# Kernel optimization log

Hardware: AMD Instinct MI355X
Metric: run time of the kernel (lower is better)

Reference implementation:

```python
import jax, jax.numpy as jnp
import numpy as np

B, C, H, W = 4, 64, 128, 128
KS = 3
N = KS * KS  # 9 sampling points per output pixel


def conv2d(x, w, stride=1, pad=0):
    return jax.lax.conv_general_dilated(
        x, w, (stride, stride), ((pad, pad), (pad, pad)),
        dimension_numbers=('NCHW', 'OIHW', 'NCHW'))


def deform_conv(x, w_p, b_p, w_m, b_m, w_c):
    """Modulated deformable conv (DCNv2, pure-pytorch DeformConv2d semantics)."""
    b, c, h, w = x.shape
    # offset: (B, 2N, H, W); mask: (B, N, H, W)
    off = conv2d(x, w_p, pad=1) + b_p[None, :, None, None]
    m = jax.nn.sigmoid(conv2d(x, w_m, pad=1) + b_m[None, :, None, None])
    # zero-pad input (padding=1), sampling coords live in padded frame
    xp = jnp.pad(x, ((0, 0), (0, 0), (1, 1), (1, 1)))
    hp, wp = h + 2, w + 2
    r = (KS - 1) // 2
    pn_x, pn_y = jnp.meshgrid(jnp.arange(-r, r + 1, dtype=x.dtype),
                              jnp.arange(-r, r + 1, dtype=x.dtype), indexing='ij')
    pn_x, pn_y = pn_x.reshape(-1), pn_y.reshape(-1)        # (N,)
    p0_x = jnp.arange(1, h + 1, dtype=x.dtype)[:, None, None]  # (H,1,1)
    p0_y = jnp.arange(1, w + 1, dtype=x.dtype)[None, :, None]  # (1,W,1)
    off_x = jnp.transpose(off[:, :N], (0, 2, 3, 1))        # (B,H,W,N)
    off_y = jnp.transpose(off[:, N:], (0, 2, 3, 1))
    px = p0_x + pn_x + off_x                               # (B,H,W,N)
    py = p0_y + pn_y + off_y
    fx, fy = jnp.floor(px), jnp.floor(py)
    q_lt_x = jnp.clip(fx, 0, hp - 1)
    q_lt_y = jnp.clip(fy, 0, wp - 1)
    q_rb_x = jnp.clip(fx + 1, 0, hp - 1)
    q_rb_y = jnp.clip(fy + 1, 0, wp - 1)
    pxc = jnp.clip(px, 0, hp - 1)
    pyc = jnp.clip(py, 0, wp - 1)
    g_lt = (1 + (q_lt_x - pxc)) * (1 + (q_lt_y - pyc))
    g_rb = (1 - (q_rb_x - pxc)) * (1 - (q_rb_y - pyc))
    g_lb = (1 + (q_lt_x - pxc)) * (1 - (q_rb_y - pyc))
    g_rt = (1 - (q_rb_x - pxc)) * (1 + (q_lt_y - pyc))
    xf = xp.reshape(b, c, hp * wp)

    def gather(xb, ix, iy):
        idx = ix.astype(jnp.int32) * wp + iy.astype(jnp.int32)  # (H,W,N)
        return xb[:, idx]                                       # (C,H,W,N)

    v_lt = jax.vmap(gather)(xf, q_lt_x, q_lt_y)
    v_rb = jax.vmap(gather)(xf, q_rb_x, q_rb_y)
    v_lb = jax.vmap(gather)(xf, q_lt_x, q_rb_y)
    v_rt = jax.vmap(gather)(xf, q_rb_x, q_lt_y)
    x_off = (g_lt[:, None] * v_lt + g_rb[:, None] * v_rb
             + g_lb[:, None] * v_lb + g_rt[:, None] * v_rt)   # (B,C,H,W,N)
    x_off = x_off * jnp.transpose(m, (0, 2, 3, 1))[:, None]   # modulation
    # (B,C,H,W,ki,kj) -> (B,C,H*KS,W*KS), then conv k=KS stride=KS, no bias
    x_off = x_off.reshape(b, c, h, w, KS, KS).transpose(0, 1, 2, 4, 3, 5)
    x_off = x_off.reshape(b, c, h * KS, w * KS)
    return conv2d(x_off, w_c, stride=KS, pad=0)


def setup_inputs() -> dict:
    key = jax.random.key(0)
    ks = jax.random.split(key, 12)
    w_scale = 1.0 / np.sqrt(C * KS * KS)
    d = {'x': jax.random.normal(ks[0], (B, C, H, W), jnp.float32)}
    for i, pre in enumerate(['d1_', 'd2_']):
        o = 1 + i * 5
        d[pre + 'w_p'] = jax.random.normal(ks[o], (2 * N, C, 3, 3), jnp.float32) * 0.02
        d[pre + 'b_p'] = jnp.zeros((2 * N,), jnp.float32)
        d[pre + 'w_m'] = jax.random.normal(ks[o + 1], (N, C, 3, 3), jnp.float32) * 0.02
        d[pre + 'b_m'] = jnp.zeros((N,), jnp.float32)
        d[pre + 'w_c'] = jax.random.normal(ks[o + 2], (C, C, KS, KS), jnp.float32) * w_scale
    return d


def reference(x, d1_w_p, d1_b_p, d1_w_m, d1_b_m, d1_w_c,
              d2_w_p, d2_b_p, d2_w_m, d2_b_m, d2_w_c):
    y = deform_conv(x, d1_w_p, d1_b_p, d1_w_m, d1_b_m, d1_w_c)
    y = jax.nn.relu(y)
    y = deform_conv(y, d2_w_p, d2_b_p, d2_w_m, d2_b_m, d2_w_c)
    return y + x
```

## Files before the change

### kernel.cpp

```cpp
#include <hip/hip_runtime.h>
#include <hip/hip_bf16.h>
#include <math.h>

typedef __attribute__((ext_vector_type(8))) short short8;
typedef __attribute__((ext_vector_type(16))) float f32x16;
typedef unsigned int uint;
typedef unsigned short ushort;

#define HWSZ 16384
#define PADW 130
#define SLAB (PADW*PADW*64)
#define WR 15
#define WC 23
#define NCELL (WR*WC)
#define CSTRIDE 144
#define OMS_OFF (NCELL*CSTRIDE)
#define SM_BYTES (OMS_OFF + 4*27*33*4)

__device__ __forceinline__ uint pk2bf(float a, float b) {
    union { __hip_bfloat162 h; uint u; } cv;
    cv.h = __float22bfloat162_rn(make_float2(a, b)); return cv.u;
}
__device__ __forceinline__ float bflo(uint u){ return __uint_as_float(u << 16); }
__device__ __forceinline__ float bfhi(uint u){ return __uint_as_float(u & 0xffff0000u); }

__device__ __forceinline__ short8 combine4(short8 s0, short8 s1, short8 s2, short8 s3,
                                           float g0, float g1, float g2, float g3)
{
    uint4 u0 = *(uint4*)&s0, u1 = *(uint4*)&s1, u2 = *(uint4*)&s2, u3 = *(uint4*)&s3;
    float v0,v1,v2,v3,v4,v5,v6,v7;
    v0 = g0*bflo(u0.x); v1 = g0*bfhi(u0.x); v2 = g0*bflo(u0.y); v3 = g0*bfhi(u0.y);
    v4 = g0*bflo(u0.z); v5 = g0*bfhi(u0.z); v6 = g0*bflo(u0.w); v7 = g0*bfhi(u0.w);
    v0 = fmaf(g1,bflo(u1.x),v0); v1 = fmaf(g1,bfhi(u1.x),v1);
    v2 = fmaf(g1,bflo(u1.y),v2); v3 = fmaf(g1,bfhi(u1.y),v3);
    v4 = fmaf(g1,bflo(u1.z),v4); v5 = fmaf(g1,bfhi(u1.z),v5);
    v6 = fmaf(g1,bflo(u1.w),v6); v7 = fmaf(g1,bfhi(u1.w),v7);
    v0 = fmaf(g2,bflo(u2.x),v0); v1 = fmaf(g2,bfhi(u2.x),v1);
    v2 = fmaf(g2,bflo(u2.y),v2); v3 = fmaf(g2,bfhi(u2.y),v3);
    v4 = fmaf(g2,bflo(u2.z),v4); v5 = fmaf(g2,bfhi(u2.z),v5);
    v6 = fmaf(g2,bflo(u2.w),v6); v7 = fmaf(g2,bfhi(u2.w),v7);
    v0 = fmaf(g3,bflo(u3.x),v0); v1 = fmaf(g3,bfhi(u3.x),v1);
    v2 = fmaf(g3,bflo(u3.y),v2); v3 = fmaf(g3,bfhi(u3.y),v3);
    v4 = fmaf(g3,bflo(u3.z),v4); v5 = fmaf(g3,bfhi(u3.z),v5);
    v6 = fmaf(g3,bflo(u3.w),v6); v7 = fmaf(g3,bfhi(u3.w),v7);
    union { short8 s; uint u[4]; } r;
    r.u[0] = pk2bf(v0,v1); r.u[1] = pk2bf(v2,v3);
    r.u[2] = pk2bf(v4,v5); r.u[3] = pk2bf(v6,v7);
    return r.s;
}

__device__ __forceinline__ void coords_tap_lds(
    const float* __restrict__ omS, int p, int irow, int jcol, int n,
    int4& cc, float4& bg)
{
    int di = n / 3, dj = n - di * 3;
    float offx = omS[n * 33 + p];
    float offy = omS[(9 + n) * 33 + p];
    float mv   = omS[(18 + n) * 33 + p];
    float pxf = (float)(irow + di) + offx;
    float pyf = (float)(jcol + dj) + offy;
    float fx = floorf(pxf), fy = floorf(pyf);
    float qltx = fminf(fmaxf(fx,       0.f), 129.f);
    float qlty = fminf(fmaxf(fy,       0.f), 129.f);
    float qrbx = fminf(fmaxf(fx + 1.f, 0.f), 129.f);
    float qrby = fminf(fmaxf(fy + 1.f, 0.f), 129.f);
    float pxc  = fminf(fmaxf(pxf,      0.f), 129.f);
    float pyc  = fminf(fmaxf(pyf,      0.f), 129.f);
    float glt = (1.f + (qltx - pxc)) * (1.f + (qlty - pyc));
    float grb = (1.f - (qrbx - pxc)) * (1.f - (qrby - pyc));
    float glb = (1.f + (qltx - pxc)) * (1.f - (qrby - pyc));
    float grt = (1.f - (qrbx - pxc)) * (1.f + (qlty - pyc));
    cc.x = (int)qltx; cc.y = (int)qlty; cc.z = (int)qrbx; cc.w = (int)qrby;
    bg.x = glt * mv; bg.y = grb * mv; bg.z = glb * mv; bg.w = grt * mv;
}

__global__ __launch_bounds__(256, 2) void prep(
    const float* __restrict__ x, ushort* __restrict__ xtt, ushort* __restrict__ y1t,
    const float* __restrict__ wc1, const float* __restrict__ wp1, const float* __restrict__ wm1,
    const float* __restrict__ wc2, const float* __restrict__ wp2, const float* __restrict__ wm2,
    ushort* __restrict__ wdf1, ushort* __restrict__ wof1,
    ushort* __restrict__ wdf2, ushort* __restrict__ wof2)
{
    int t = threadIdx.x;
    if (blockIdx.x < 432) {
        int idx0 = blockIdx.x * 256 + t;
        union { __hip_bfloat16 h; ushort u; } cv;
        if (idx0 < 73728) {
            int lay = idx0 >= 36864;
            int idx = idx0 - lay * 36864;
            const float* wc = lay ? wc2 : wc1;
            ushort* dst = lay ? wdf2 : wdf1;
            int j = idx & 7, l = (idx >> 3) & 63;
            int nt = (idx >> 9) & 1, kb = (idx >> 10) & 3, tap = idx >> 12;
            int oc = nt * 32 + (l & 31);
            int c  = kb * 16 + ((l >> 5) << 3) + j;
            cv.h = __float2bfloat16(wc[(oc * 64 + c) * 9 + tap]);
            dst[idx] = cv.u;
        } else if (idx0 < 110592) {
            int r = idx0 - 73728;
            int lay = r >= 18432;
            int idx = r - lay * 18432;
            const float* wp = lay ? wp2 : wp1;
            const float* wm = lay ? wm2 : wm1;
            ushort* dst = lay ? wof2 : wof1;
            int j = idx & 7, l = (idx >> 3) & 63;
            int kb = (idx >> 9) & 3, tap = idx >> 11;
            int ch = l & 31;
            int c  = kb * 16 + ((l >> 5) << 3) + j;
            float v = 0.f;
            if (ch < 18)      v = wp[(ch * 64 + c) * 9 + tap];
            else if (ch < 27) v = wm[((ch - 18) * 64 + c) * 9 + tap];
            cv.h = __float2bfloat16(v);
            dst[idx] = cv.u;
        }
        return;
    }
    int bx = blockIdx.x - 432;
    int l = t & 63, wv = t >> 6;
    if (bx < 128) {
        int c2 = l & 31, ps = l >> 5;
        int pix0w = bx * 512 + wv * 128;
        int bq = pix0w >> 14;
        const float* xp0 = x + ((size_t)(bq * 64 + c2 * 2)) * HWSZ;
        ushort* xw = xtt + (size_t)bq * SLAB;
        #pragma unroll 8
        for (int p = 0; p < 64; ++p) {
            int pxi = (pix0w + p * 2 + ps) & (HWSZ - 1);
            int i = pxi >> 7, j = pxi & 127;
            uint u = pk2bf(xp0[pxi], xp0[pxi + HWSZ]);
            *(uint*)(xw + ((i + 1) * PADW + (j + 1)) * 64 + c2 * 2) = u;
        }
    } else {
        int idx = (bx - 128) * 256 + t;
        if (idx >= 264192) return;
        ushort* buf = (idx >= 132096) ? y1t : xtt;
        int e_all = idx % 132096;
        int bq = e_all / 33024, e = e_all % 33024;
        int i, j, c;
        if (e < 8320)       { i = 0;   j = e >> 6; c = e & 63; }
        else if (e < 16640) { int e2 = e - 8320; i = 129; j = e2 >> 6; c = e2 & 63; }
        else                { int e2 = e - 16640; c = e2 & 63;
                              i = (e2 >> 7) + 1; j = ((e2 >> 6) & 1) ? 129 : 0; }
        buf[(size_t)bq * SLAB + (i * PADW + j) * 64 + c] = 0;
    }
}

#define MF32(a,b,c) __builtin_amdgcn_mfma_f32_32x32x16_bf16(a,b,c,0,0,0)

__global__ __launch_bounds__(256, 2) void fused(
    const ushort* __restrict__ xt, const ushort* __restrict__ wof,
    const float* __restrict__ bp, const float* __restrict__ bm,
    const ushort* __restrict__ wdf, const float* __restrict__ xres,
    float* __restrict__ outn, ushort* __restrict__ y1t, int mode)
{
    __shared__ __align__(16) char sm[SM_BYTES];
    const int t = threadIdx.x, l = t & 63, wv = t >> 6;
    const int lb = (blockIdx.x & 7) * 64 + (blockIdx.x >> 3);
    const int bb = lb >> 7;
    const int patch = lb & 127;
    const int i0 = (patch >> 3) * 8;
    const int j0 = (patch & 7) * 16;
    const int p  = l & 31;
    const int h5 = l >> 5;
    const ushort* xb = xt + (size_t)bb * SLAB;
    const char* xbb = (const char*)xb;

    for (int s = t; s < NCELL * 8; s += 256) {
        int q = s & 7, cq = s >> 3;
        int c = cq % WC, r = cq / WC;
        int ip = min(max(i0 - 2 + r, 0), 129);
        int jp = min(max(j0 - 2 + c, 0), 129);
        uint4 v = *(const uint4*)(xbb + ((ip * PADW + jp) << 7) + (q << 4));
        *(uint4*)(sm + cq * CSTRIDE + (q << 4)) = v;
    }
    __syncthreads();

    f32x16 oacc = {0.f,0.f,0.f,0.f,0.f,0.f,0.f,0.f,0.f,0.f,0.f,0.f,0.f,0.f,0.f,0.f};
    {
        const int rbase = 2 * wv + (p >> 4) + 2;
        const int cbase = (p & 15) + 2;
        #pragma unroll
        for (int tap = 0; tap < 9; ++tap) {
            int ti = tap / 3, tj = tap - ti * 3;
            const char* cell = sm + ((rbase + ti) * WC + cbase + tj) * CSTRIDE;
            #pragma unroll
            for (int kb = 0; kb < 4; ++kb) {
                short8 b = *(const short8*)(wof + ((tap * 4 + kb) * 64 + l) * 8);
                short8 a = *(const short8*)(cell + ((kb * 2 + h5) << 4));
                oacc = MF32(a, b, oacc);
            }
        }
    }
    float* omS = (float*)(sm + OMS_OFF) + wv * 891;
    {
        int ch = l & 31;
        if (ch < 27) {
            float bias = (ch < 18) ? bp[ch] : bm[ch - 18];
            #pragma unroll
            for (int reg = 0; reg < 16; ++reg) {
                int m = (reg & 3) + 8 * (reg >> 2) + 4 * h5;
                float v = oacc[reg] + bias;
                if (ch >= 18) v = 1.f / (1.f + __expf(-v));
                omS[ch * 33 + m] = v;
            }
        }
    }

    f32x16 acc0 = {0.f,0.f,0.f,0.f,0.f,0.f,0.f,0.f,0.f,0.f,0.f,0.f,0.f,0.f,0.f,0.f};
    f32x16 acc1 = acc0;
    const int irow = i0 + 2 * wv + (p >> 4), jcol = j0 + (p & 15);
    uint cpack[9]; float4 gw[9];
    bool okall = true;
    #pragma unroll
    for (int n = 0; n < 9; ++n) {
        int4 cc; float4 g;
        coords_tap_lds(omS, p, irow, jcol, n, cc, g);
        int rlt = cc.x - (i0 - 2), clt = cc.y - (j0 - 2);
        int rrb = cc.z - (i0 - 2), crb = cc.w - (j0 - 2);
        okall = okall & ((uint)rlt < (uint)WR) & ((uint)rrb < (uint)WR) &
                        ((uint)clt < (uint)WC) & ((uint)crb < (uint)WC);
        cpack[n] = (uint)(rlt & 255) | ((uint)(clt & 255) << 8) |
                   ((uint)(rrb & 255) << 16) | ((uint)(crb & 255) << 24);
        gw[n] = g;
    }

    if (__all(okall)) {
        #pragma unroll
        for (int n = 0; n < 9; ++n) {
            uint cp_ = cpack[n];
            int rlt = cp_ & 255, clt = (cp_ >> 8) & 255;
            int rrb = (cp_ >> 16) & 255, crb = cp_ >> 24;
            const char* bLT = sm + (rlt * WC + clt) * CSTRIDE;
            const char* bRB = sm + (rrb * WC + crb) * CSTRIDE;
            const char* bLB = sm + (rlt * WC + crb) * CSTRIDE;
            const char* bRT = sm + (rrb * WC + clt) * CSTRIDE;
            float4 g = gw[n];
            const ushort* wb = wdf + (size_t)n * 4096 + l * 8;
            #pragma unroll
            for (int kb = 0; kb < 4; ++kb) {
                int qo = (kb * 2 + h5) << 4;
                short8 w0 = *(const short8*)(wb + (kb * 2 + 0) * 512);
                short8 w1 = *(const short8*)(wb + (kb * 2 + 1) * 512);
                short8 sLT = *(const short8*)(bLT + qo);
                short8 sRB = *(const short8*)(bRB + qo);
                short8 sLB = *(const short8*)(bLB + qo);
                short8 sRT = *(const short8*)(bRT + qo);
                short8 a = combine4(sLT, sRB, sLB, sRT, g.x, g.y, g.z, g.w);
                acc0 = MF32(a, w0, acc0);
                acc1 = MF32(a, w1, acc1);
            }
        }
    } else {
        #pragma unroll
        for (int n = 0; n < 9; ++n) {
            int4 cc; float4 g;
            coords_tap_lds(omS, p, irow, jcol, n, cc, g);
            int rlt = cc.x - (i0 - 2), clt = cc.y - (j0 - 2);
            int rrb = cc.z - (i0 - 2), crb = cc.w - (j0 - 2);
            bool ok = ((uint)rlt < (uint)WR) & ((uint)rrb < (uint)WR) &
                      ((uint)clt < (uint)WC) & ((uint)crb < (uint)WC);
            const ushort* wb = wdf + (size_t)n * 4096 + l * 8;
            #pragma unroll
            for (int kb = 0; kb < 4; ++kb) {
                int qo = (kb * 2 + h5) << 4;
                short8 w0 = *(const short8*)(wb + (kb * 2 + 0) * 512);
                short8 w1 = *(const short8*)(wb + (kb * 2 + 1) * 512);
                short8 sLT, sRB, sLB, sRT;
                if (ok) {
                    sLT = *(const short8*)(sm + (rlt * WC + clt) * CSTRIDE + qo);
                    sRB = *(const short8*)(sm + (rrb * WC + crb) * CSTRIDE + qo);
                    sLB = *(const short8*)(sm + (rlt * WC + crb) * CSTRIDE + qo);
                    sRT = *(const short8*)(sm + (rrb * WC + clt) * CSTRIDE + qo);
                } else {
                    sLT = *(const short8*)(xbb + (((cc.x * PADW + cc.y) << 7) + qo));
                    sRB = *(const short8*)(xbb + (((cc.z * PADW + cc.w) << 7) + qo));
                    sLB = *(const short8*)(xbb + (((cc.x * PADW + cc.w) << 7) + qo));
                    sRT = *(const short8*)(xbb + (((cc.z * PADW + cc.y) << 7) + qo));
                }
                short8 a = combine4(sLT, sRB, sLB, sRT, g.x, g.y, g.z, g.w);
                acc0 = MF32(a, w0, acc0);
                acc1 = MF32(a, w1, acc1);
            }
        }
    }

    if (mode == 0) {
        #pragma unroll
        for (int nt = 0; nt < 2; ++nt) {
            int oc = nt * 32 + (l & 31);
            const f32x16& av = nt ? acc1 : acc0;
            #pragma unroll
            for (int qd = 0; qd < 4; ++qd) {
                int m0 = 8 * qd + 4 * h5;
                int lr = m0 >> 4, col0 = m0 & 15;
                size_t o = ((size_t)(bb * 64 + oc)) * HWSZ +
                           (i0 + 2 * wv + lr) * 128 + j0 + col0;
                float4 rsd = *(const float4*)(xres + o);
                float4 vv;
                vv.x = av[qd * 4 + 0] + rsd.x; vv.y = av[qd * 4 + 1] + rsd.y;
                vv.z = av[qd * 4 + 2] + rsd.z; vv.w = av[qd * 4 + 3] + rsd.w;
                *(float4*)(outn + o) = vv;
            }
        }
    } else {
        __syncthreads();
        float* T = (float*)sm;
        #pragma unroll
        for (int nt = 0; nt < 2; ++nt) {
            int oc = nt * 32 + (l & 31);
            const f32x16& av = nt ? acc1 : acc0;
            #pragma unroll
            for (int reg = 0; reg < 16; ++reg) {
                int m = (reg & 3) + 8 * (reg >> 2) + 4 * h5;
                int plin = (2 * wv + (m >> 4)) * 16 + (m & 15);
                T[oc * 129 + plin] = fmaxf(av[reg], 0.f);
            }
        }
        __syncthreads();
        int plin = t >> 1, och = (t & 1) * 32;
        int prow = plin >> 4, pcol = plin & 15;
        ushort* dst = y1t + (size_t)bb * SLAB +
                      ((i0 + prow + 1) * PADW + (j0 + pcol + 1)) * 64 + och;
        uint w[16];
        #pragma unroll
        for (int k2 = 0; k2 < 16; ++k2)
            w[k2] = pk2bf(T[(och + k2 * 2) * 129 + plin],
                          T[(och + k2 * 2 + 1) * 129 + plin]);
        *(uint4*)dst        = make_uint4(w[0],  w[1],  w[2],  w[3]);
        *(uint4*)(dst + 8)  = make_uint4(w[4],  w[5],  w[6],  w[7]);
        *(uint4*)(dst + 16) = make_uint4(w[8],  w[9],  w[10], w[11]);
        *(uint4*)(dst + 24) = make_uint4(w[12], w[13], w[14], w[15]);
    }
}

extern "C" void kernel_launch(void* const* d_in, const int* in_sizes, int n_in,
                              void* d_out, int out_size, void* d_ws, size_t ws_size,
                              hipStream_t stream)
{
    const float* x      = (const float*)d_in[0];
    const float* d1_w_p = (const float*)d_in[1];
    const float* d1_b_p = (const float*)d_in[2];
    const float* d1_w_m = (const float*)d_in[3];
    const float* d1_b_m = (const float*)d_in[4];
    const float* d1_w_c = (const float*)d_in[5];
    const float* d2_w_p = (const float*)d_in[6];
    const float* d2_b_p = (const float*)d_in[7];
    const float* d2_w_m = (const float*)d_in[8];
    const float* d2_b_m = (const float*)d_in[9];
    const float* d2_w_c = (const float*)d_in[10];
    float* out = (float*)d_out;

    char* ws = (char*)d_ws;
    ushort* xtt  = (ushort*)(ws);
    ushort* y1t  = (ushort*)(ws + 8652800);
    ushort* wdf1 = (ushort*)(ws + 17305600);
    ushort* wof1 = (ushort*)(ws + 17379328);
    ushort* wdf2 = (ushort*)(ws + 17416192);
    ushort* wof2 = (ushort*)(ws + 17489920);

    prep<<<1592, 256, 0, stream>>>(x, xtt, y1t,
                                   d1_w_c, d1_w_p, d1_w_m, d2_w_c, d2_w_p, d2_w_m,
                                   wdf1, wof1, wdf2, wof2);

    fused<<<512, 256, 0, stream>>>(xtt, wof1, d1_b_p, d1_b_m, wdf1,
                                   nullptr, nullptr, y1t, 1);
    fused<<<512, 256, 0, stream>>>(y1t, wof2, d2_b_p, d2_b_m, wdf2,
                                   x, out, nullptr, 0);
}
```

Before: 73.66 us.

## XOR-swizzle LDS cell layout and write layer-1 output directly without LDS transpose

Applies an XOR swizzle on the 16-byte chunks within each LDS cell, keyed by cell index, to reduce bank conflicts in the offset-conv and bilinear gather reads. Also removes the LDS transpose stage and its two barriers for the mode-1 output, writing each bf16 value straight to global memory as a scattered 2-byte store. The direct writes avoid the syncs and LDS traffic but produce many small, poorly coalesced global stores.

```diff
diff --git a/kernel.cpp b/kernel.cpp
--- a/kernel.cpp
+++ b/kernel.cpp
@@ -17,9 +17,17 @@
 #define OMS_OFF (NCELL*CSTRIDE)
 #define SM_BYTES (OMS_OFF + 4*27*33*4)
 
+__device__ __forceinline__ int hx16(int ci) {
+    return ((ci ^ (ci >> 3)) & 7) << 4;
+}
+
 __device__ __forceinline__ uint pk2bf(float a, float b) {
     union { __hip_bfloat162 h; uint u; } cv;
     cv.h = __float22bfloat162_rn(make_float2(a, b)); return cv.u;
+}
+__device__ __forceinline__ ushort f2bfu(float a) {
+    union { __hip_bfloat16 h; ushort u; } cv;
+    cv.h = __float2bfloat16(a); return cv.u;
 }
 __device__ __forceinline__ float bflo(uint u){ return __uint_as_float(u << 16); }
 __device__ __forceinline__ float bfhi(uint u){ return __uint_as_float(u & 0xffff0000u); }
@@ -171,7 +179,7 @@
         int ip = min(max(i0 - 2 + r, 0), 129);
         int jp = min(max(j0 - 2 + c, 0), 129);
         uint4 v = *(const uint4*)(xbb + ((ip * PADW + jp) << 7) + (q << 4));
-        *(uint4*)(sm + cq * CSTRIDE + (q << 4)) = v;
+        *(uint4*)(sm + cq * CSTRIDE + ((q << 4) ^ hx16(cq))) = v;
     }
     __syncthreads();
 
@@ -182,11 +190,13 @@
         #pragma unroll
         for (int tap = 0; tap < 9; ++tap) {
             int ti = tap / 3, tj = tap - ti * 3;
-            const char* cell = sm + ((rbase + ti) * WC + cbase + tj) * CSTRIDE;
+            int ci = (rbase + ti) * WC + cbase + tj;
+            const char* cell = sm + ci * CSTRIDE;
+            int hb = hx16(ci);
             #pragma unroll
             for (int kb = 0; kb < 4; ++kb) {
                 short8 b = *(const short8*)(wof + ((tap * 4 + kb) * 64 + l) * 8);
-                short8 a = *(const short8*)(cell + ((kb * 2 + h5) << 4));
+                short8 a = *(const short8*)(cell + (((kb * 2 + h5) << 4) ^ hb));
                 oacc = MF32(a, b, oacc);
             }
         }
@@ -230,10 +240,14 @@
             uint cp_ = cpack[n];
             int rlt = cp_ & 255, clt = (cp_ >> 8) & 255;
             int rrb = (cp_ >> 16) & 255, crb = cp_ >> 24;
-            const char* bLT = sm + (rlt * WC + clt) * CSTRIDE;
-            const char* bRB = sm + (rrb * WC + crb) * CSTRIDE;
-            const char* bLB = sm + (rlt * WC + crb) * CSTRIDE;
-            const char* bRT = sm + (rrb * WC + clt) * CSTRIDE;
+            int ciLT = rlt * WC + clt, ciRB = rrb * WC + crb;
+            int ciLB = rlt * WC + crb, ciRT = rrb * WC + clt;
+            const char* bLT = sm + ciLT * CSTRIDE;
+            const char* bRB = sm + ciRB * CSTRIDE;
+            const char* bLB = sm + ciLB * CSTRIDE;
+            const char* bRT = sm + ciRT * CSTRIDE;
+            int hLT = hx16(ciLT), hRB = hx16(ciRB);
+            int hLB = hx16(ciLB), hRT = hx16(ciRT);
             float4 g = gw[n];
             const ushort* wb = wdf + (size_t)n * 4096 + l * 8;
             #pragma unroll
@@ -241,10 +255,10 @@
                 int qo = (kb * 2 + h5) << 4;
                 short8 w0 = *(const short8*)(wb + (kb * 2 + 0) * 512);
                 short8 w1 = *(const short8*)(wb + (kb * 2 + 1) * 512);
-                short8 sLT = *(const short8*)(bLT + qo);
-                short8 sRB = *(const short8*)(bRB + qo);
-                short8 sLB = *(const short8*)(bLB + qo);
-                short8 sRT = *(const short8*)(bRT + qo);
+                short8 sLT = *(const short8*)(bLT + (qo ^ hLT));
+                short8 sRB = *(const short8*)(bRB + (qo ^ hRB));
+                short8 sLB = *(const short8*)(bLB + (qo ^ hLB));
+                short8 sRT = *(const short8*)(bRT + (qo ^ hRT));
                 short8 a = combine4(sLT, sRB, sLB, sRT, g.x, g.y, g.z, g.w);
                 acc0 = MF32(a, w0, acc0);
                 acc1 = MF32(a, w1, acc1);
@@ -267,10 +281,12 @@
                 short8 w1 = *(const short8*)(wb + (kb * 2 + 1) * 512);
                 short8 sLT, sRB, sLB, sRT;
                 if (ok) {
-                    sLT = *(const short8*)(sm + (rlt * WC + clt) * CSTRIDE + qo);
-                    sRB = *(const short8*)(sm + (rrb * WC + crb) * CSTRIDE + qo);
-                    sLB = *(const short8*)(sm + (rlt * WC + crb) * CSTRIDE + qo);
-                    sRT = *(const short8*)(sm + (rrb * WC + clt) * CSTRIDE + qo);
+                    int ciLT = rlt * WC + clt, ciRB = rrb * WC + crb;
+                    int ciLB = rlt * WC + crb, ciRT = rrb * WC + clt;
+                    sLT = *(const short8*)(sm + ciLT * CSTRIDE + (qo ^ hx16(ciLT)));
+                    sRB = *(const short8*)(sm + ciRB * CSTRIDE + (qo ^ hx16(ciRB)));
+                    sLB = *(const short8*)(sm + ciLB * CSTRIDE + (qo ^ hx16(ciLB)));
+                    sRT = *(const short8*)(sm + ciRT * CSTRIDE + (qo ^ hx16(ciRT)));
                 } else {
                     sLT = *(const short8*)(xbb + (((cc.x * PADW + cc.y) << 7) + qo));
                     sRB = *(const short8*)(xbb + (((cc.z * PADW + cc.w) << 7) + qo));
@@ -303,8 +319,7 @@
             }
         }
     } else {
-        __syncthreads();
-        float* T = (float*)sm;
+        ushort* yb = y1t + (size_t)bb * SLAB;
         #pragma unroll
         for (int nt = 0; nt < 2; ++nt) {
             int oc = nt * 32 + (l & 31);
@@ -312,24 +327,11 @@
             #pragma unroll
             for (int reg = 0; reg < 16; ++reg) {
                 int m = (reg & 3) + 8 * (reg >> 2) + 4 * h5;
-                int plin = (2 * wv + (m >> 4)) * 16 + (m & 15);
-                T[oc * 129 + plin] = fmaxf(av[reg], 0.f);
-            }
-        }
-        __syncthreads();
-        int plin = t >> 1, och = (t & 1) * 32;
-        int prow = plin >> 4, pcol = plin & 15;
-        ushort* dst = y1t + (size_t)bb * SLAB +
-                      ((i0 + prow + 1) * PADW + (j0 + pcol + 1)) * 64 + och;
-        uint w[16];
-        #pragma unroll
-        for (int k2 = 0; k2 < 16; ++k2)
-            w[k2] = pk2bf(T[(och + k2 * 2) * 129 + plin],
-                          T[(och + k2 * 2 + 1) * 129 + plin]);
-        *(uint4*)dst        = make_uint4(w[0],  w[1],  w[2],  w[3]);
-        *(uint4*)(dst + 8)  = make_uint4(w[4],  w[5],  w[6],  w[7]);
-        *(uint4*)(dst + 16) = make_uint4(w[8],  w[9],  w[10], w[11]);
-        *(uint4*)(dst + 24) = make_uint4(w[12], w[13], w[14], w[15]);
+                int ip = i0 + 2 * wv + (m >> 4) + 1;
+                int jp = j0 + (m & 15) + 1;
+                yb[(ip * PADW + jp) * 64 + oc] = f2bfu(fmaxf(av[reg], 0.f));
+            }
+        }
     }
 }
 
```

Measured after the change: 74.07 us. Within noise of the previous version (+0.6%).
